# Performance work log

Hardware: AMD Instinct MI355X
Metric: run time of the kernel (lower is better)

Reference implementation:

```python
import jax, jax.numpy as jnp
import numpy as np

NEG_SLOPE = 0.2


def gat_layer(x, src, dst, W, a_src, a_dst, b, n_nodes):
    # x: [N, F_in]; W: [F_in, H*C]; a_src/a_dst: [H, C]; b: [H*C]
    H, C = a_src.shape
    h = (x @ W).reshape(n_nodes, H, C)                    # [N, H, C]
    al_s = jnp.sum(h * a_src, axis=-1)                    # [N, H]
    al_d = jnp.sum(h * a_dst, axis=-1)                    # [N, H]
    e = jax.nn.leaky_relu(al_s[src] + al_d[dst], NEG_SLOPE)  # [E, H]
    # segment softmax over incoming edges of each dst node
    m = jax.ops.segment_max(e, dst, num_segments=n_nodes)   # [N, H]
    e = jnp.exp(e - m[dst])
    s = jax.ops.segment_sum(e, dst, num_segments=n_nodes)   # [N, H]
    alpha = e / (s[dst] + 1e-16)                             # [E, H]
    msg = h[src] * alpha[:, :, None]                         # [E, H, C]
    out = jax.ops.segment_sum(msg, dst, num_segments=n_nodes)
    return out.reshape(n_nodes, H * C) + b


def setup_inputs() -> dict:
    key = jax.random.key(0)
    ks = jax.random.split(key, 16)
    N, E = 50000, 800000
    F_in, Hd, heads, n_cls = 256, 256, 8, 64
    C = Hd // heads
    x = jax.random.normal(ks[0], (N, F_in), dtype=jnp.float32)
    edge_index = jax.random.randint(ks[1], (2, E), 0, N, dtype=jnp.int64)

    def lin(k, fin, fout):
        return jax.random.normal(k, (fin, fout), dtype=jnp.float32) / np.sqrt(fin).astype(np.float32)

    inp = {"x": x, "edge_index": edge_index}
    # layer 1: 256 -> 8 heads x 32
    inp["W1"] = lin(ks[2], F_in, Hd)
    inp["as1"] = jax.random.normal(ks[3], (heads, C), dtype=jnp.float32) * 0.1
    inp["ad1"] = jax.random.normal(ks[4], (heads, C), dtype=jnp.float32) * 0.1
    inp["b1"] = jnp.zeros((Hd,), dtype=jnp.float32)
    # layer 2: 256 -> 8 heads x 32
    inp["W2"] = lin(ks[5], Hd, Hd)
    inp["as2"] = jax.random.normal(ks[6], (heads, C), dtype=jnp.float32) * 0.1
    inp["ad2"] = jax.random.normal(ks[7], (heads, C), dtype=jnp.float32) * 0.1
    inp["b2"] = jnp.zeros((Hd,), dtype=jnp.float32)
    # layer 3: 256 -> 1 head x 64 (num_classes)
    inp["W3"] = lin(ks[8], Hd, n_cls)
    inp["as3"] = jax.random.normal(ks[9], (1, n_cls), dtype=jnp.float32) * 0.1
    inp["ad3"] = jax.random.normal(ks[10], (1, n_cls), dtype=jnp.float32) * 0.1
    inp["b3"] = jnp.zeros((n_cls,), dtype=jnp.float32)
    return inp


def reference(x, edge_index, W1, as1, ad1, b1, W2, as2, ad2, b2, W3, as3, ad3, b3):
    N = x.shape[0]
    # PyG GATConv default add_self_loops=True
    loop = jnp.arange(N, dtype=edge_index.dtype)
    src = jnp.concatenate([edge_index[0], loop])
    dst = jnp.concatenate([edge_index[1], loop])
    h = gat_layer(x, src, dst, W1, as1, ad1, b1, N)
    h = jax.nn.relu(h)  # dropout is identity at inference
    h = gat_layer(h, src, dst, W2, as2, ad2, b2, N)
    h = jax.nn.relu(h)
    out = gat_layer(h, src, dst, W3, as3, ad3, b3, N)
    return out
```

## Files before the change

### kernel.cpp

```cpp
#include <hip/hip_runtime.h>
#include <math.h>

#define NSLOPE 0.2f

typedef __attribute__((ext_vector_type(8))) short bf16x8;
typedef __attribute__((ext_vector_type(8))) unsigned short ushort8;
typedef __attribute__((ext_vector_type(4))) float f32x4;

static __device__ __forceinline__ float leaky(float e) {
    return e > 0.f ? e : NSLOPE * e;
}

static __device__ __forceinline__ float bfu(unsigned short u) {
    return __uint_as_float(((unsigned)u) << 16);
}

static __device__ __forceinline__ unsigned short f2bf_rne(float f) {
    unsigned b = __float_as_uint(f);
    unsigned r = b + 0x7fffu + ((b >> 16) & 1u);
    return (unsigned short)(r >> 16);
}

static __device__ __forceinline__ void split1(float f, unsigned short& hi,
                                              unsigned short& lo) {
    unsigned b = __float_as_uint(f);
    unsigned hb = b & 0xffff0000u;
    hi = (unsigned short)(hb >> 16);
    lo = (unsigned short)(__float_as_uint(f - __uint_as_float(hb)) >> 16);
}


__global__ void k_count(const int* __restrict__ dst, int* __restrict__ cnt, int E) {
    int i = blockIdx.x * blockDim.x + threadIdx.x;
    if (i < E) atomicAdd(&cnt[dst[i]], 1);
}

__global__ void k_scan_local(const int* __restrict__ cnt, int* __restrict__ ptr,
                             int* __restrict__ bsum, int N) {
    __shared__ int sd[256];
    int t = threadIdx.x;
    int i0 = blockIdx.x * 1024 + t * 4;
    int v0 = (i0 + 0 < N) ? cnt[i0 + 0] : 0;
    int v1 = (i0 + 1 < N) ? cnt[i0 + 1] : 0;
    int v2 = (i0 + 2 < N) ? cnt[i0 + 2] : 0;
    int v3 = (i0 + 3 < N) ? cnt[i0 + 3] : 0;
    int ts = v0 + v1 + v2 + v3;
    sd[t] = ts;
    __syncthreads();
    for (int o = 1; o < 256; o <<= 1) {
        int add = (t >= o) ? sd[t - o] : 0;
        __syncthreads();
        sd[t] += add;
        __syncthreads();
    }
    int run = sd[t] - ts;
    if (i0 + 0 < N) ptr[i0 + 0] = run; run += v0;
    if (i0 + 1 < N) ptr[i0 + 1] = run; run += v1;
    if (i0 + 2 < N) ptr[i0 + 2] = run; run += v2;
    if (i0 + 3 < N) ptr[i0 + 3] = run;
    if (t == 255) bsum[blockIdx.x] = sd[255];
}

__global__ void k_scan_add2(int* __restrict__ ptr, const int* __restrict__ bsum,
                            int N, int Et) {
    __shared__ int base;
    const int chunk = blockIdx.x >> 2;
    if (threadIdx.x == 0) {
        int s = 0;
        for (int b = 0; b < chunk; ++b) s += bsum[b];
        base = s;
    }
    __syncthreads();
    int i = blockIdx.x * 256 + threadIdx.x;
    if (i < N) ptr[i] += base;
    else if (i == N) ptr[N] = Et;
}

__global__ void k_copy(int* __restrict__ d, const int* __restrict__ s, int N) {
    int i = blockIdx.x * blockDim.x + threadIdx.x;
    if (i < N) d[i] = s[i];
}

__global__ void k_fillcsr(const int* __restrict__ ei, int* __restrict__ fptr,
                          int* __restrict__ srcs, int E, int Et) {
    int i = blockIdx.x * blockDim.x + threadIdx.x;
    if (i >= Et) return;
    int s, d;
    if (i < E) { s = ei[i]; d = ei[E + i]; }
    else       { s = d = i - E; }
    int pos = atomicAdd(&fptr[d], 1);
    srcs[pos] = s;
}

__global__ __launch_bounds__(256) void k_prep(
    int* __restrict__ cnt, int N,
    const float* __restrict__ x, unsigned short* __restrict__ xhi,
    unsigned short* __restrict__ xlo, int n8,
    const float* __restrict__ W1, unsigned short* __restrict__ w1h, unsigned short* __restrict__ w1l,
    const float* __restrict__ W2, unsigned short* __restrict__ w2h, unsigned short* __restrict__ w2l,
    const float* __restrict__ W3, unsigned short* __restrict__ w3h, unsigned short* __restrict__ w3l,
    int nset, int nsplit) {
    __shared__ float tile[32][33];
    const int b = blockIdx.x;
    const int tid = threadIdx.x;
    if (b < nset) {
        int i = b * 256 + tid;
        if (i < N) cnt[i] = 1;
    } else if (b < nset + nsplit) {
        int i = (b - nset) * 256 + tid;
        if (i < n8) {
            const float4 v0 = *reinterpret_cast<const float4*>(&x[(size_t)i * 8]);
            const float4 v1 = *reinterpret_cast<const float4*>(&x[(size_t)i * 8 + 4]);
            const float f[8] = {v0.x, v0.y, v0.z, v0.w, v1.x, v1.y, v1.z, v1.w};
            ushort8 h, l;
#pragma unroll
            for (int j = 0; j < 8; ++j) {
                unsigned short hj, lj;
                split1(f[j], hj, lj);
                h[j] = hj; l[j] = lj;
            }
            *reinterpret_cast<ushort8*>(&xhi[(size_t)i * 8]) = h;
            *reinterpret_cast<ushort8*>(&xlo[(size_t)i * 8]) = l;
        }
    } else {
        int tb = b - nset - nsplit;
        const float* B; unsigned short *H, *L;
        int M, bx, by;
        if (tb < 64)       { B = W1; H = w1h; L = w1l; M = 256; bx = (tb & 7) * 32; by = (tb >> 3) * 32; }
        else if (tb < 128) { tb -= 64;  B = W2; H = w2h; L = w2l; M = 256; bx = (tb & 7) * 32; by = (tb >> 3) * 32; }
        else               { tb -= 128; B = W3; H = w3h; L = w3l; M = 64;  bx = (tb & 1) * 32; by = (tb >> 1) * 32; }
        constexpr int K = 256;
        const int tx = tid & 31, ty = tid >> 5;
        for (int r = ty; r < 32; r += 8) tile[r][tx] = B[(size_t)(by + r) * M + bx + tx];
        __syncthreads();
        for (int r = ty; r < 32; r += 8) {
            unsigned short h, l;
            split1(tile[tx][r], h, l);
            H[(size_t)(bx + r) * K + by + tx] = h;
            L[(size_t)(bx + r) * K + by + tx] = l;
        }
    }
}

__global__ __launch_bounds__(256) void k_gemm2(const unsigned short* __restrict__ Ahi,
                                               const unsigned short* __restrict__ Alo,
                                               const unsigned short* __restrict__ Whi,
                                               const unsigned short* __restrict__ Wlo,
                                               const float* __restrict__ asrc,
                                               const float* __restrict__ adst,
                                               unsigned short* __restrict__ hb,
                                               float* __restrict__ als,
                                               float* __restrict__ ald,
                                               int N) {
    constexpr int K = 256;
    constexpr int M = 256;
    __shared__ unsigned short Ah[64][36], Al[64][36];
    __shared__ unsigned short Bh[256][36], Bl[256][36];
    const int tid = threadIdx.x;
    const int lane = tid & 63;
    const int wid = tid >> 6;
    const int row0 = blockIdx.x * 64;

    const int sr = tid >> 2;
    const int sk = (tid & 3) << 3;
    const int ga = row0 + sr;
    const size_t gaK = (size_t)ga * K;

    const int wc0 = wid * 64;
    const int fr = lane & 15;
    const int ko = (lane >> 4) * 8;

    f32x4 acc[4][4];
#pragma unroll
    for (int i = 0; i < 4; ++i)
#pragma unroll
        for (int j = 0; j < 4; ++j) acc[i][j] = (f32x4){0.f, 0.f, 0.f, 0.f};

    for (int k0 = 0; k0 < K; k0 += 32) {
        ushort8 ah = {0,0,0,0,0,0,0,0}, al = {0,0,0,0,0,0,0,0};
        if (ga < N) {
            ah = *reinterpret_cast<const ushort8*>(&Ahi[gaK + k0 + sk]);
            al = *reinterpret_cast<const ushort8*>(&Alo[gaK + k0 + sk]);
        }
        *reinterpret_cast<ushort8*>(&Ah[sr][sk]) = ah;
        *reinterpret_cast<ushort8*>(&Al[sr][sk]) = al;
#pragma unroll
        for (int p = 0; p < 4; ++p) {
            const int m = sr + 64 * p;
            const size_t gm = (size_t)m * K + k0 + sk;
            *reinterpret_cast<ushort8*>(&Bh[m][sk]) =
                *reinterpret_cast<const ushort8*>(&Whi[gm]);
            *reinterpret_cast<ushort8*>(&Bl[m][sk]) =
                *reinterpret_cast<const ushort8*>(&Wlo[gm]);
        }
        __syncthreads();

        bf16x8 ahi[4], alo4[4];
#pragma unroll
        for (int i = 0; i < 4; ++i) {
            ahi[i]  = *reinterpret_cast<const bf16x8*>(&Ah[i * 16 + fr][ko]);
            alo4[i] = *reinterpret_cast<const bf16x8*>(&Al[i * 16 + fr][ko]);
        }
#pragma unroll
        for (int j = 0; j < 4; ++j) {
            const bf16x8 bh = *reinterpret_cast<const bf16x8*>(&Bh[wc0 + j * 16 + fr][ko]);
            const bf16x8 bl = *reinterpret_cast<const bf16x8*>(&Bl[wc0 + j * 16 + fr][ko]);
#pragma unroll
            for (int i = 0; i < 4; ++i) {
                acc[i][j] = __builtin_amdgcn_mfma_f32_16x16x32_bf16(ahi[i], bh, acc[i][j], 0, 0, 0);
                acc[i][j] = __builtin_amdgcn_mfma_f32_16x16x32_bf16(ahi[i], bl, acc[i][j], 0, 0, 0);
                acc[i][j] = __builtin_amdgcn_mfma_f32_16x16x32_bf16(alo4[i], bh, acc[i][j], 0, 0, 0);
            }
        }
        __syncthreads();
    }

    const int orow = (lane >> 4) * 4;
    const int ocol = lane & 15;

#pragma unroll
    for (int i = 0; i < 4; ++i) {
#pragma unroll
        for (int r = 0; r < 4; ++r) {
            const int row = row0 + i * 16 + orow + r;
            if (row < N) {
#pragma unroll
                for (int j = 0; j < 4; ++j) {
                    const int col = wc0 + j * 16 + ocol;
                    hb[(size_t)row * M + col] = f2bf_rne(acc[i][j][r]);
                }
            }
        }
    }

    const float as0 = asrc[wc0 + ocol],      as1 = asrc[wc0 + 16 + ocol];
    const float as2 = asrc[wc0 + 32 + ocol], as3 = asrc[wc0 + 48 + ocol];
    const float ad0 = adst[wc0 + ocol],      ad1 = adst[wc0 + 16 + ocol];
    const float ad2 = adst[wc0 + 32 + ocol], ad3 = adst[wc0 + 48 + ocol];
    const int headA = wc0 >> 5, headB = headA + 1;

#pragma unroll
    for (int i = 0; i < 4; ++i) {
#pragma unroll
        for (int r = 0; r < 4; ++r) {
            float psA = acc[i][0][r] * as0 + acc[i][1][r] * as1;
            float pdA = acc[i][0][r] * ad0 + acc[i][1][r] * ad1;
            float psB = acc[i][2][r] * as2 + acc[i][3][r] * as3;
            float pdB = acc[i][2][r] * ad2 + acc[i][3][r] * ad3;
#pragma unroll
            for (int o = 1; o < 16; o <<= 1) {
                psA += __shfl_xor(psA, o);
                pdA += __shfl_xor(pdA, o);
                psB += __shfl_xor(psB, o);
                pdB += __shfl_xor(pdB, o);
            }
            const int row = row0 + i * 16 + orow + r;
            if (ocol == 0 && row < N) {
                als[(size_t)row * 8 + headA] = psA;
                ald[(size_t)row * 8 + headA] = pdA;
                als[(size_t)row * 8 + headB] = psB;
                ald[(size_t)row * 8 + headB] = pdB;
            }
        }
    }
}


template <int HN, int CN>
__global__ __launch_bounds__(256) void k_gemm_s(const unsigned short* __restrict__ Ahi,
                                                const unsigned short* __restrict__ Alo,
                                                const unsigned short* __restrict__ Whi,
                                                const unsigned short* __restrict__ Wlo,
                                                const float* __restrict__ asrc,
                                                const float* __restrict__ adst,
                                                unsigned short* __restrict__ hb,
                                                float* __restrict__ als,
                                                float* __restrict__ ald,
                                                int N) {
    constexpr int K = 256;
    constexpr int M = HN * CN;
    __shared__ unsigned short Ah[64][40], Al[64][40], Bh[64][40], Bl[64][40];
    const int tid = threadIdx.x;
    const int lane = tid & 63;
    const int wid = tid >> 6;
    const int row0 = blockIdx.x * 64;
    const int col0 = blockIdx.y * 64;

    const int sr = tid >> 2;
    const int sk = (tid & 3) << 3;
    const int ga = row0 + sr;
    const size_t gaK = (size_t)ga * K;
    const size_t gcK = (size_t)(col0 + sr) * K;

    const int wr = (wid >> 1) * 32;
    const int wc = (wid & 1) * 32;
    const int fr = lane & 15;
    const int ko = (lane >> 4) * 8;

    f32x4 acc[2][2];
#pragma unroll
    for (int i = 0; i < 2; ++i)
#pragma unroll
        for (int j = 0; j < 2; ++j) acc[i][j] = (f32x4){0.f, 0.f, 0.f, 0.f};

    for (int k0 = 0; k0 < K; k0 += 32) {
        ushort8 ah = {0,0,0,0,0,0,0,0}, al = {0,0,0,0,0,0,0,0};
        if (ga < N) {
            ah = *reinterpret_cast<const ushort8*>(&Ahi[gaK + k0 + sk]);
            al = *reinterpret_cast<const ushort8*>(&Alo[gaK + k0 + sk]);
        }
        const ushort8 bh = *reinterpret_cast<const ushort8*>(&Whi[gcK + k0 + sk]);
        const ushort8 bl = *reinterpret_cast<const ushort8*>(&Wlo[gcK + k0 + sk]);
        *reinterpret_cast<ushort8*>(&Ah[sr][sk]) = ah;
        *reinterpret_cast<ushort8*>(&Al[sr][sk]) = al;
        *reinterpret_cast<ushort8*>(&Bh[sr][sk]) = bh;
        *reinterpret_cast<ushort8*>(&Bl[sr][sk]) = bl;
        __syncthreads();

        bf16x8 ahi[2], alo[2], bhi[2], blo[2];
#pragma unroll
        for (int i = 0; i < 2; ++i) {
            ahi[i] = *reinterpret_cast<const bf16x8*>(&Ah[wr + i * 16 + fr][ko]);
            alo[i] = *reinterpret_cast<const bf16x8*>(&Al[wr + i * 16 + fr][ko]);
        }
#pragma unroll
        for (int j = 0; j < 2; ++j) {
            bhi[j] = *reinterpret_cast<const bf16x8*>(&Bh[wc + j * 16 + fr][ko]);
            blo[j] = *reinterpret_cast<const bf16x8*>(&Bl[wc + j * 16 + fr][ko]);
        }
#pragma unroll
        for (int i = 0; i < 2; ++i)
#pragma unroll
            for (int j = 0; j < 2; ++j) {
                acc[i][j] = __builtin_amdgcn_mfma_f32_16x16x32_bf16(ahi[i], bhi[j], acc[i][j], 0, 0, 0);
                acc[i][j] = __builtin_amdgcn_mfma_f32_16x16x32_bf16(ahi[i], blo[j], acc[i][j], 0, 0, 0);
                acc[i][j] = __builtin_amdgcn_mfma_f32_16x16x32_bf16(alo[i], bhi[j], acc[i][j], 0, 0, 0);
            }
        __syncthreads();
    }

    const int orow = (lane >> 4) * 4;
    const int ocol = lane & 15;

#pragma unroll
    for (int i = 0; i < 2; ++i) {
#pragma unroll
        for (int r = 0; r < 4; ++r) {
            const int row = row0 + wr + i * 16 + orow + r;
            if (row < N) {
#pragma unroll
                for (int j = 0; j < 2; ++j) {
                    const int col = col0 + wc + j * 16 + ocol;
                    hb[(size_t)row * M + col] = f2bf_rne(acc[i][j][r]);
                }
            }
        }
    }

    const int c0 = col0 + wc;
    const float as0 = asrc[c0 + ocol],      as1 = asrc[c0 + 16 + ocol];
    const float ad0 = adst[c0 + ocol],      ad1 = adst[c0 + 16 + ocol];

    {
        __shared__ float part[2][64][2];
#pragma unroll
        for (int i = 0; i < 2; ++i) {
#pragma unroll
            for (int r = 0; r < 4; ++r) {
                float ps = acc[i][0][r] * as0 + acc[i][1][r] * as1;
                float pd = acc[i][0][r] * ad0 + acc[i][1][r] * ad1;
#pragma unroll
                for (int o = 1; o < 16; o <<= 1) {
                    ps += __shfl_xor(ps, o);
                    pd += __shfl_xor(pd, o);
                }
                if (ocol == 0) {
                    const int lr = wr + i * 16 + orow + r;
                    part[wc >> 5][lr][0] = ps;
                    part[wc >> 5][lr][1] = pd;
                }
            }
        }
        __syncthreads();
        if (tid < 64) {
            const int row = row0 + tid;
            if (row < N) {
                als[row] = part[0][tid][0] + part[1][tid][0];
                ald[row] = part[0][tid][1] + part[1][tid][1];
            }
        }
    }
}

template <int HN, int CN, int VEC, int P, bool OSPLIT>
__global__ __launch_bounds__(256) void k_agg6(const unsigned short* __restrict__ hb,
                                              const float* __restrict__ als,
                                              const float* __restrict__ ald,
                                              const int* __restrict__ ptr,
                                              const int* __restrict__ srcs,
                                              const float* __restrict__ bias,
                                              unsigned short* __restrict__ ohi,
                                              unsigned short* __restrict__ olo,
                                              float* __restrict__ out,
                                              int N, int relu) {
    constexpr int HC = HN * CN;
    constexpr int SUBS = 64 / HN;
    constexpr int GB = (SUBS < 16) ? SUBS : 16;
    const int l = threadIdx.x & 63;
    const int n = blockIdx.x * 4 + (threadIdx.x >> 6);
    if (n >= N) return;
    const int beg = ptr[n], end = ptr[n + 1];
    const int hd_e = l % HN;
    const int sub = l / HN;
    const float aldv = ald[(unsigned)n * HN + hd_e];

    float p[P];
    int   sr[P];
    float ssum = 0.f;
#pragma unroll
    for (int b = 0; b < P; ++b) {
        const int j = beg + b * SUBS + sub;
        float pv = 0.f; int s = 0;
        if (j < end) {
            s = srcs[j];
            pv = __expf(leaky(als[(unsigned)s * HN + hd_e] + aldv));
        }
        sr[b] = s; p[b] = pv; ssum += pv;
    }
    for (int j = beg + P * SUBS + sub; j < end; j += SUBS) {
        ssum += __expf(leaky(als[(unsigned)srcs[j] * HN + hd_e] + aldv));
    }
#pragma unroll
    for (int o = HN; o < 64; o <<= 1) ssum += __shfl_xor(ssum, o);
    const float inv = 1.f / (ssum + 1e-16f);

    const int ch = l * VEC;
    const int hl = ch / CN;
    float acc[VEC];
#pragma unroll
    for (int v = 0; v < VEC; ++v) acc[v] = 0.f;

#pragma unroll
    for (int b = 0; b < P; ++b) {
        const int j0 = beg + b * SUBS;
        if (j0 >= end) break;
        const float am = p[b] * inv;
#pragma unroll
        for (int cb = 0; cb < SUBS / GB; ++cb) {
            if (j0 + cb * GB >= end) break;
            float av[GB];
            if constexpr (VEC == 4) {
                ushort4 hv[GB];
#pragma unroll
                for (int c = 0; c < GB; ++c) {
                    const int ce = cb * GB + c;
                    const int s = __shfl(sr[b], ce * HN);
                    av[c] = __shfl(am, ce * HN + hl);
                    hv[c] = *reinterpret_cast<const ushort4*>(&hb[(unsigned)s * HC + ch]);
                }
#pragma unroll
                for (int c = 0; c < GB; ++c) {
                    acc[0] += av[c] * bfu(hv[c].x);
                    acc[1] += av[c] * bfu(hv[c].y);
                    acc[2] += av[c] * bfu(hv[c].z);
                    acc[3] += av[c] * bfu(hv[c].w);
                }
            } else {
                unsigned short hv[GB];
#pragma unroll
                for (int c = 0; c < GB; ++c) {
                    const int ce = cb * GB + c;
                    const int s = __shfl(sr[b], ce * HN);
                    av[c] = __shfl(am, ce * HN + hl);
                    hv[c] = hb[(unsigned)s * HC + ch];
                }
#pragma unroll
                for (int c = 0; c < GB; ++c) acc[0] += av[c] * bfu(hv[c]);
            }
        }
    }
    for (int j0 = beg + P * SUBS; j0 < end; j0 += SUBS) {
        const int j = j0 + sub;
        int sm = 0; float am = 0.f;
        if (j < end) {
            sm = srcs[j];
            am = __expf(leaky(als[(unsigned)sm * HN + hd_e] + aldv)) * inv;
        }
#pragma unroll
        for (int cb = 0; cb < SUBS / GB; ++cb) {
            if (j0 + cb * GB >= end) break;
            float av[GB];
            if constexpr (VEC == 4) {
                ushort4 hv[GB];
#pragma unroll
                for (int c = 0; c < GB; ++c) {
                    const int ce = cb * GB + c;
                    const int s = __shfl(sm, ce * HN);
                    av[c] = __shfl(am, ce * HN + hl);
                    hv[c] = *reinterpret_cast<const ushort4*>(&hb[(unsigned)s * HC + ch]);
                }
#pragma unroll
                for (int c = 0; c < GB; ++c) {
                    acc[0] += av[c] * bfu(hv[c].x);
                    acc[1] += av[c] * bfu(hv[c].y);
                    acc[2] += av[c] * bfu(hv[c].z);
                    acc[3] += av[c] * bfu(hv[c].w);
                }
            } else {
                unsigned short hv[GB];
#pragma unroll
                for (int c = 0; c < GB; ++c) {
                    const int ce = cb * GB + c;
                    const int s = __shfl(sm, ce * HN);
                    av[c] = __shfl(am, ce * HN + hl);
                    hv[c] = hb[(unsigned)s * HC + ch];
                }
#pragma unroll
                for (int c = 0; c < GB; ++c) acc[0] += av[c] * bfu(hv[c]);
            }
        }
    }

#pragma unroll
    for (int v = 0; v < VEC; ++v) {
        float o = acc[v] + bias[ch + v];
        if (relu) o = fmaxf(o, 0.f);
        acc[v] = o;
    }
    if constexpr (OSPLIT) {
        ushort4 ho, lo4;
        unsigned short h0, l0;
        split1(acc[0], h0, l0); ho.x = h0; lo4.x = l0;
        split1(acc[1], h0, l0); ho.y = h0; lo4.y = l0;
        split1(acc[2], h0, l0); ho.z = h0; lo4.z = l0;
        split1(acc[3], h0, l0); ho.w = h0; lo4.w = l0;
        *reinterpret_cast<ushort4*>(&ohi[(unsigned)n * HC + ch]) = ho;
        *reinterpret_cast<ushort4*>(&olo[(unsigned)n * HC + ch]) = lo4;
    } else if constexpr (VEC == 4) {
        float4 vout;
        vout.x = acc[0]; vout.y = acc[1]; vout.z = acc[2]; vout.w = acc[3];
        *reinterpret_cast<float4*>(&out[(unsigned)n * HC + ch]) = vout;
    } else {
        out[(unsigned)n * HC + ch] = acc[0];
    }
}

template <int P>
__global__ __launch_bounds__(256) void k_agg7(const unsigned short* __restrict__ hb,
                                              const float* __restrict__ als,
                                              const float* __restrict__ ald,
                                              const int* __restrict__ ptr,
                                              const int* __restrict__ srcs,
                                              const float* __restrict__ bias,
                                              float* __restrict__ out,
                                              int N) {
    constexpr int HC = 64;
    const int l = threadIdx.x & 63;
    const int n = blockIdx.x * 4 + (threadIdx.x >> 6);
    if (n >= N) return;
    const int beg = ptr[n], end = ptr[n + 1];
    const float aldv = ald[n];

    float p[P];
    int   sr[P];
    float ssum = 0.f;
#pragma unroll
    for (int b = 0; b < P; ++b) {
        const int j = beg + b * 64 + l;
        float pv = 0.f; int s = 0;
        if (j < end) { s = srcs[j]; pv = __expf(leaky(als[s] + aldv)); }
        sr[b] = s; p[b] = pv; ssum += pv;
    }
    for (int j = beg + P * 64 + l; j < end; j += 64)
        ssum += __expf(leaky(als[srcs[j]] + aldv));
#pragma unroll
    for (int o = 1; o < 64; o <<= 1) ssum += __shfl_xor(ssum, o);
    const float inv = 1.f / (ssum + 1e-16f);

    const int grp = l >> 4;
    const int lch = (l & 15) * 4;
    float acc[4] = {0.f, 0.f, 0.f, 0.f};

#pragma unroll
    for (int b = 0; b < P; ++b) {
        const int j0 = beg + b * 64;
        if (j0 >= end) break;
        const float am = p[b] * inv;
        const int ned = min(64, end - j0);
        const int nblk = (ned + 15) >> 4;
        for (int cb = 0; cb < nblk; ++cb) {
            const int e0 = cb * 16 + grp;
            const float a0 = __shfl(am, e0),       a1 = __shfl(am, e0 + 4);
            const float a2 = __shfl(am, e0 + 8),   a3 = __shfl(am, e0 + 12);
            const int   s0 = __shfl(sr[b], e0),      s1 = __shfl(sr[b], e0 + 4);
            const int   s2 = __shfl(sr[b], e0 + 8),  s3 = __shfl(sr[b], e0 + 12);
            const ushort4 h0 = *reinterpret_cast<const ushort4*>(&hb[(unsigned)s0 * HC + lch]);
            const ushort4 h1 = *reinterpret_cast<const ushort4*>(&hb[(unsigned)s1 * HC + lch]);
            const ushort4 h2 = *reinterpret_cast<const ushort4*>(&hb[(unsigned)s2 * HC + lch]);
            const ushort4 h3 = *reinterpret_cast<const ushort4*>(&hb[(unsigned)s3 * HC + lch]);
            acc[0] += a0 * bfu(h0.x) + a1 * bfu(h1.x) + a2 * bfu(h2.x) + a3 * bfu(h3.x);
            acc[1] += a0 * bfu(h0.y) + a1 * bfu(h1.y) + a2 * bfu(h2.y) + a3 * bfu(h3.y);
            acc[2] += a0 * bfu(h0.z) + a1 * bfu(h1.z) + a2 * bfu(h2.z) + a3 * bfu(h3.z);
            acc[3] += a0 * bfu(h0.w) + a1 * bfu(h1.w) + a2 * bfu(h2.w) + a3 * bfu(h3.w);
        }
    }
    for (int j0 = beg + P * 64; j0 < end; j0 += 64) {
        const int j = j0 + l;
        int sm = 0; float am = 0.f;
        if (j < end) { sm = srcs[j]; am = __expf(leaky(als[sm] + aldv)) * inv; }
        const int ned = min(64, end - j0);
        const int nblk = (ned + 15) >> 4;
        for (int cb = 0; cb < nblk; ++cb) {
            const int e0 = cb * 16 + grp;
            const float a0 = __shfl(am, e0),       a1 = __shfl(am, e0 + 4);
            const float a2 = __shfl(am, e0 + 8),   a3 = __shfl(am, e0 + 12);
            const int   s0 = __shfl(sm, e0),       s1 = __shfl(sm, e0 + 4);
            const int   s2 = __shfl(sm, e0 + 8),   s3 = __shfl(sm, e0 + 12);
            const ushort4 h0 = *reinterpret_cast<const ushort4*>(&hb[(unsigned)s0 * HC + lch]);
            const ushort4 h1 = *reinterpret_cast<const ushort4*>(&hb[(unsigned)s1 * HC + lch]);
            const ushort4 h2 = *reinterpret_cast<const ushort4*>(&hb[(unsigned)s2 * HC + lch]);
            const ushort4 h3 = *reinterpret_cast<const ushort4*>(&hb[(unsigned)s3 * HC + lch]);
            acc[0] += a0 * bfu(h0.x) + a1 * bfu(h1.x) + a2 * bfu(h2.x) + a3 * bfu(h3.x);
            acc[1] += a0 * bfu(h0.y) + a1 * bfu(h1.y) + a2 * bfu(h2.y) + a3 * bfu(h3.y);
            acc[2] += a0 * bfu(h0.z) + a1 * bfu(h1.z) + a2 * bfu(h2.z) + a3 * bfu(h3.z);
            acc[3] += a0 * bfu(h0.w) + a1 * bfu(h1.w) + a2 * bfu(h2.w) + a3 * bfu(h3.w);
        }
    }

#pragma unroll
    for (int o = 16; o < 64; o <<= 1) {
#pragma unroll
        for (int v = 0; v < 4; ++v) acc[v] += __shfl_xor(acc[v], o);
    }

    if (l < 16) {
        float4 vout;
        vout.x = acc[0] + bias[lch + 0];
        vout.y = acc[1] + bias[lch + 1];
        vout.z = acc[2] + bias[lch + 2];
        vout.w = acc[3] + bias[lch + 3];
        *reinterpret_cast<float4*>(&out[(size_t)n * HC + lch]) = vout;
    }
}


extern "C" void kernel_launch(void* const* d_in, const int* in_sizes, int n_in,
                              void* d_out, int out_size, void* d_ws, size_t ws_size,
                              hipStream_t stream) {
    const float* x   = (const float*)d_in[0];
    const int*   ei  = (const int*)d_in[1];
    const float* W1  = (const float*)d_in[2];
    const float* as1 = (const float*)d_in[3];
    const float* ad1 = (const float*)d_in[4];
    const float* b1  = (const float*)d_in[5];
    const float* W2  = (const float*)d_in[6];
    const float* as2 = (const float*)d_in[7];
    const float* ad2 = (const float*)d_in[8];
    const float* b2  = (const float*)d_in[9];
    const float* W3  = (const float*)d_in[10];
    const float* as3 = (const float*)d_in[11];
    const float* ad3 = (const float*)d_in[12];
    const float* b3  = (const float*)d_in[13];

    const int F  = 256;
    const int N  = in_sizes[0] / F;
    const int E  = in_sizes[1] / 2;
    const int Et = E + N;

    char* w = (char*)d_ws;
    auto alloc = [&](size_t bytes) {
        char* p = w;
        w += (bytes + 255) & ~(size_t)255;
        return p;
    };
    unsigned short* S0hi = (unsigned short*)alloc((size_t)N * F * 2);
    unsigned short* S0lo = (unsigned short*)alloc((size_t)N * F * 2);
    unsigned short* S1hi = (unsigned short*)alloc((size_t)N * F * 2);
    unsigned short* S1lo = (unsigned short*)alloc((size_t)N * F * 2);
    unsigned short* hB   = (unsigned short*)alloc((size_t)N * F * 2);
    unsigned short* Wt1hi = (unsigned short*)alloc((size_t)256 * 256 * 2);
    unsigned short* Wt1lo = (unsigned short*)alloc((size_t)256 * 256 * 2);
    unsigned short* Wt2hi = (unsigned short*)alloc((size_t)256 * 256 * 2);
    unsigned short* Wt2lo = (unsigned short*)alloc((size_t)256 * 256 * 2);
    unsigned short* Wt3hi = (unsigned short*)alloc((size_t)64 * 256 * 2);
    unsigned short* Wt3lo = (unsigned short*)alloc((size_t)64 * 256 * 2);
    float* als  = (float*)alloc((size_t)N * 8 * 4);
    float* ald  = (float*)alloc((size_t)N * 8 * 4);
    int*   cnt  = (int*)alloc((size_t)N * 4);
    int*   ptr  = (int*)alloc((size_t)(N + 1) * 4);
    int*   fptr = (int*)alloc((size_t)(N + 1) * 4);
    int*   srcs = (int*)alloc((size_t)Et * 4);
    int*   bsum = (int*)alloc(4096);

    const int n8 = N * F / 8;
    const int nset = (N + 255) / 256;
    const int nsplit = (n8 + 255) / 256;
    const int nprep = nset + nsplit + 64 + 64 + 16;

    hipLaunchKernelGGL(k_prep, dim3(nprep), dim3(256), 0, stream,
                       cnt, N, x, S0hi, S0lo, n8,
                       W1, Wt1hi, Wt1lo, W2, Wt2hi, Wt2lo, W3, Wt3hi, Wt3lo,
                       nset, nsplit);

    const int nb = (N + 1023) / 1024;
    hipLaunchKernelGGL(k_count,     dim3((E + 255) / 256),  dim3(256), 0, stream, ei + E, cnt, E);
    hipLaunchKernelGGL(k_scan_local,dim3(nb),               dim3(256), 0, stream, cnt, ptr, bsum, N);
    hipLaunchKernelGGL(k_scan_add2, dim3((N + 256) / 256),  dim3(256), 0, stream, ptr, bsum, N, Et);
    hipLaunchKernelGGL(k_copy,      dim3((N + 255) / 256),  dim3(256), 0, stream, fptr, ptr, N);
    hipLaunchKernelGGL(k_fillcsr,   dim3((Et + 255) / 256), dim3(256), 0, stream, ei, fptr, srcs, E, Et);

    const dim3 gN4((N + 3) / 4);
    const int gx = (N + 63) / 64;

    hipLaunchKernelGGL(k_gemm2, dim3(gx), dim3(256), 0, stream,
                       S0hi, S0lo, Wt1hi, Wt1lo, as1, ad1, hB, als, ald, N);
    hipLaunchKernelGGL((k_agg6<8, 32, 4, 8, true>), gN4, dim3(256), 0, stream,
                       hB, als, ald, ptr, srcs, b1, S1hi, S1lo, nullptr, N, 1);
    hipLaunchKernelGGL(k_gemm2, dim3(gx), dim3(256), 0, stream,
                       S1hi, S1lo, Wt2hi, Wt2lo, as2, ad2, hB, als, ald, N);
    hipLaunchKernelGGL((k_agg6<8, 32, 4, 8, true>), gN4, dim3(256), 0, stream,
                       hB, als, ald, ptr, srcs, b2, S0hi, S0lo, nullptr, N, 1);
    hipLaunchKernelGGL((k_gemm_s<1, 64>), dim3(gx, 1), dim3(256), 0, stream,
                       S0hi, S0lo, Wt3hi, Wt3lo, as3, ad3, hB, als, ald, N);
    hipLaunchKernelGGL((k_agg7<2>), gN4, dim3(256), 0, stream,
                       hB, als, ald, ptr, srcs, b3, (float*)d_out, N);
}
```

Measured before the change: 381.1 us.

## Use 16-byte gathers with half-wave edge split in GAT aggregation; fuse ptr copy

The 8-head aggregation kernel now has each lane load 8 bf16 channels (16 bytes) per source row instead of 4. The wave is split into two 32-lane halves that each process alternate edges, and a cross-half shuffle reduces the partial sums before write-out. This aims to halve the number of gather instructions and raise bytes per load on the irregular neighbor gathers, at the cost of an extra shuffle reduction and idle upper lanes during the store. Separately, the fptr copy is folded into the scan-add kernel, which removes one launch.

```diff
diff --git a/kernel.cpp b/kernel.cpp
--- a/kernel.cpp
+++ b/kernel.cpp
@@ -61,8 +61,8 @@
     if (t == 255) bsum[blockIdx.x] = sd[255];
 }
 
-__global__ void k_scan_add2(int* __restrict__ ptr, const int* __restrict__ bsum,
-                            int N, int Et) {
+__global__ void k_scan_add2(int* __restrict__ ptr, int* __restrict__ fptr,
+                            const int* __restrict__ bsum, int N, int Et) {
     __shared__ int base;
     const int chunk = blockIdx.x >> 2;
     if (threadIdx.x == 0) {
@@ -72,13 +72,13 @@
     }
     __syncthreads();
     int i = blockIdx.x * 256 + threadIdx.x;
-    if (i < N) ptr[i] += base;
-    else if (i == N) ptr[N] = Et;
-}
-
-__global__ void k_copy(int* __restrict__ d, const int* __restrict__ s, int N) {
-    int i = blockIdx.x * blockDim.x + threadIdx.x;
-    if (i < N) d[i] = s[i];
+    if (i < N) {
+        int v = ptr[i] + base;
+        ptr[i] = v;
+        fptr[i] = v;
+    } else if (i == N) {
+        ptr[N] = Et;
+    }
 }
 
 __global__ void k_fillcsr(const int* __restrict__ ei, int* __restrict__ fptr,
@@ -392,8 +392,8 @@
     }
 }
 
-template <int HN, int CN, int VEC, int P, bool OSPLIT>
-__global__ __launch_bounds__(256) void k_agg6(const unsigned short* __restrict__ hb,
+template <int P, bool OSPLIT>
+__global__ __launch_bounds__(256) void k_agg8(const unsigned short* __restrict__ hb,
                                               const float* __restrict__ als,
                                               const float* __restrict__ ald,
                                               const int* __restrict__ ptr,
@@ -403,145 +403,108 @@
                                               unsigned short* __restrict__ olo,
                                               float* __restrict__ out,
                                               int N, int relu) {
-    constexpr int HC = HN * CN;
-    constexpr int SUBS = 64 / HN;
-    constexpr int GB = (SUBS < 16) ? SUBS : 16;
+    constexpr int HC = 256;
     const int l = threadIdx.x & 63;
     const int n = blockIdx.x * 4 + (threadIdx.x >> 6);
     if (n >= N) return;
     const int beg = ptr[n], end = ptr[n + 1];
-    const int hd_e = l % HN;
-    const int sub = l / HN;
-    const float aldv = ald[(unsigned)n * HN + hd_e];
+    const int hd_e = l & 7;
+    const int sub = l >> 3;
+    const float aldv = ald[(unsigned)n * 8 + hd_e];
 
     float p[P];
     int   sr[P];
     float ssum = 0.f;
 #pragma unroll
     for (int b = 0; b < P; ++b) {
-        const int j = beg + b * SUBS + sub;
+        const int j = beg + b * 8 + sub;
         float pv = 0.f; int s = 0;
         if (j < end) {
             s = srcs[j];
-            pv = __expf(leaky(als[(unsigned)s * HN + hd_e] + aldv));
+            pv = __expf(leaky(als[(unsigned)s * 8 + hd_e] + aldv));
         }
         sr[b] = s; p[b] = pv; ssum += pv;
     }
-    for (int j = beg + P * SUBS + sub; j < end; j += SUBS) {
-        ssum += __expf(leaky(als[(unsigned)srcs[j] * HN + hd_e] + aldv));
-    }
-#pragma unroll
-    for (int o = HN; o < 64; o <<= 1) ssum += __shfl_xor(ssum, o);
+    for (int j = beg + P * 8 + sub; j < end; j += 8) {
+        ssum += __expf(leaky(als[(unsigned)srcs[j] * 8 + hd_e] + aldv));
+    }
+#pragma unroll
+    for (int o = 8; o < 64; o <<= 1) ssum += __shfl_xor(ssum, o);
     const float inv = 1.f / (ssum + 1e-16f);
 
-    const int ch = l * VEC;
-    const int hl = ch / CN;
-    float acc[VEC];
-#pragma unroll
-    for (int v = 0; v < VEC; ++v) acc[v] = 0.f;
+    const int grp = l >> 5;
+    const int lch = (l & 31) * 8;
+    const int hl = (l & 31) >> 2;
+    float acc[8];
+#pragma unroll
+    for (int v = 0; v < 8; ++v) acc[v] = 0.f;
 
 #pragma unroll
     for (int b = 0; b < P; ++b) {
-        const int j0 = beg + b * SUBS;
+        const int j0 = beg + b * 8;
         if (j0 >= end) break;
         const float am = p[b] * inv;
-#pragma unroll
-        for (int cb = 0; cb < SUBS / GB; ++cb) {
-            if (j0 + cb * GB >= end) break;
-            float av[GB];
-            if constexpr (VEC == 4) {
-                ushort4 hv[GB];
-#pragma unroll
-                for (int c = 0; c < GB; ++c) {
-                    const int ce = cb * GB + c;
-                    const int s = __shfl(sr[b], ce * HN);
-                    av[c] = __shfl(am, ce * HN + hl);
-                    hv[c] = *reinterpret_cast<const ushort4*>(&hb[(unsigned)s * HC + ch]);
-                }
-#pragma unroll
-                for (int c = 0; c < GB; ++c) {
-                    acc[0] += av[c] * bfu(hv[c].x);
-                    acc[1] += av[c] * bfu(hv[c].y);
-                    acc[2] += av[c] * bfu(hv[c].z);
-                    acc[3] += av[c] * bfu(hv[c].w);
-                }
-            } else {
-                unsigned short hv[GB];
-#pragma unroll
-                for (int c = 0; c < GB; ++c) {
-                    const int ce = cb * GB + c;
-                    const int s = __shfl(sr[b], ce * HN);
-                    av[c] = __shfl(am, ce * HN + hl);
-                    hv[c] = hb[(unsigned)s * HC + ch];
-                }
-#pragma unroll
-                for (int c = 0; c < GB; ++c) acc[0] += av[c] * bfu(hv[c]);
-            }
-        }
-    }
-    for (int j0 = beg + P * SUBS; j0 < end; j0 += SUBS) {
+        float a[4]; int s[4]; ushort8 hv[4];
+#pragma unroll
+        for (int k = 0; k < 4; ++k) {
+            const int ce = 2 * k + grp;
+            a[k] = __shfl(am, ce * 8 + hl);
+            s[k] = __shfl(sr[b], ce * 8);
+            hv[k] = *reinterpret_cast<const ushort8*>(&hb[(unsigned)s[k] * HC + lch]);
+        }
+#pragma unroll
+        for (int k = 0; k < 4; ++k)
+#pragma unroll
+            for (int v = 0; v < 8; ++v) acc[v] += a[k] * bfu(hv[k][v]);
+    }
+    for (int j0 = beg + P * 8; j0 < end; j0 += 8) {
         const int j = j0 + sub;
         int sm = 0; float am = 0.f;
         if (j < end) {
             sm = srcs[j];
-            am = __expf(leaky(als[(unsigned)sm * HN + hd_e] + aldv)) * inv;
-        }
-#pragma unroll
-        for (int cb = 0; cb < SUBS / GB; ++cb) {
-            if (j0 + cb * GB >= end) break;
-            float av[GB];
-            if constexpr (VEC == 4) {
-                ushort4 hv[GB];
-#pragma unroll
-                for (int c = 0; c < GB; ++c) {
-                    const int ce = cb * GB + c;
-                    const int s = __shfl(sm, ce * HN);
-                    av[c] = __shfl(am, ce * HN + hl);
-                    hv[c] = *reinterpret_cast<const ushort4*>(&hb[(unsigned)s * HC + ch]);
-                }
-#pragma unroll
-                for (int c = 0; c < GB; ++c) {
-                    acc[0] += av[c] * bfu(hv[c].x);
-                    acc[1] += av[c] * bfu(hv[c].y);
-                    acc[2] += av[c] * bfu(hv[c].z);
-                    acc[3] += av[c] * bfu(hv[c].w);
-                }
-            } else {
-                unsigned short hv[GB];
-#pragma unroll
-                for (int c = 0; c < GB; ++c) {
-                    const int ce = cb * GB + c;
-                    const int s = __shfl(sm, ce * HN);
-                    av[c] = __shfl(am, ce * HN + hl);
-                    hv[c] = hb[(unsigned)s * HC + ch];
-                }
-#pragma unroll
-                for (int c = 0; c < GB; ++c) acc[0] += av[c] * bfu(hv[c]);
-            }
-        }
-    }
-
-#pragma unroll
-    for (int v = 0; v < VEC; ++v) {
-        float o = acc[v] + bias[ch + v];
-        if (relu) o = fmaxf(o, 0.f);
-        acc[v] = o;
-    }
-    if constexpr (OSPLIT) {
-        ushort4 ho, lo4;
-        unsigned short h0, l0;
-        split1(acc[0], h0, l0); ho.x = h0; lo4.x = l0;
-        split1(acc[1], h0, l0); ho.y = h0; lo4.y = l0;
-        split1(acc[2], h0, l0); ho.z = h0; lo4.z = l0;
-        split1(acc[3], h0, l0); ho.w = h0; lo4.w = l0;
-        *reinterpret_cast<ushort4*>(&ohi[(unsigned)n * HC + ch]) = ho;
-        *reinterpret_cast<ushort4*>(&olo[(unsigned)n * HC + ch]) = lo4;
-    } else if constexpr (VEC == 4) {
-        float4 vout;
-        vout.x = acc[0]; vout.y = acc[1]; vout.z = acc[2]; vout.w = acc[3];
-        *reinterpret_cast<float4*>(&out[(unsigned)n * HC + ch]) = vout;
-    } else {
-        out[(unsigned)n * HC + ch] = acc[0];
+            am = __expf(leaky(als[(unsigned)sm * 8 + hd_e] + aldv)) * inv;
+        }
+        float a[4]; int s[4]; ushort8 hv[4];
+#pragma unroll
+        for (int k = 0; k < 4; ++k) {
+            const int ce = 2 * k + grp;
+            a[k] = __shfl(am, ce * 8 + hl);
+            s[k] = __shfl(sm, ce * 8);
+            hv[k] = *reinterpret_cast<const ushort8*>(&hb[(unsigned)s[k] * HC + lch]);
+        }
+#pragma unroll
+        for (int k = 0; k < 4; ++k)
+#pragma unroll
+            for (int v = 0; v < 8; ++v) acc[v] += a[k] * bfu(hv[k][v]);
+    }
+
+#pragma unroll
+    for (int v = 0; v < 8; ++v) acc[v] += __shfl_xor(acc[v], 32);
+
+    if (l < 32) {
+#pragma unroll
+        for (int v = 0; v < 8; ++v) {
+            float o = acc[v] + bias[lch + v];
+            if (relu) o = fmaxf(o, 0.f);
+            acc[v] = o;
+        }
+        if constexpr (OSPLIT) {
+            ushort8 ho, lo8;
+#pragma unroll
+            for (int v = 0; v < 8; ++v) {
+                unsigned short h0, l0;
+                split1(acc[v], h0, l0);
+                ho[v] = h0; lo8[v] = l0;
+            }
+            *reinterpret_cast<ushort8*>(&ohi[(unsigned)n * HC + lch]) = ho;
+            *reinterpret_cast<ushort8*>(&olo[(unsigned)n * HC + lch]) = lo8;
+        } else {
+            float4 v0, v1;
+            v0.x = acc[0]; v0.y = acc[1]; v0.z = acc[2]; v0.w = acc[3];
+            v1.x = acc[4]; v1.y = acc[5]; v1.z = acc[6]; v1.w = acc[7];
+            *reinterpret_cast<float4*>(&out[(unsigned)n * HC + lch]) = v0;
+            *reinterpret_cast<float4*>(&out[(unsigned)n * HC + lch + 4]) = v1;
+        }
     }
 }
 
@@ -705,8 +668,7 @@
     const int nb = (N + 1023) / 1024;
     hipLaunchKernelGGL(k_count,     dim3((E + 255) / 256),  dim3(256), 0, stream, ei + E, cnt, E);
     hipLaunchKernelGGL(k_scan_local,dim3(nb),               dim3(256), 0, stream, cnt, ptr, bsum, N);
-    hipLaunchKernelGGL(k_scan_add2, dim3((N + 256) / 256),  dim3(256), 0, stream, ptr, bsum, N, Et);
-    hipLaunchKernelGGL(k_copy,      dim3((N + 255) / 256),  dim3(256), 0, stream, fptr, ptr, N);
+    hipLaunchKernelGGL(k_scan_add2, dim3((N + 256) / 256),  dim3(256), 0, stream, ptr, fptr, bsum, N, Et);
     hipLaunchKernelGGL(k_fillcsr,   dim3((Et + 255) / 256), dim3(256), 0, stream, ei, fptr, srcs, E, Et);
 
     const dim3 gN4((N + 3) / 4);
@@ -714,11 +676,11 @@
 
     hipLaunchKernelGGL(k_gemm2, dim3(gx), dim3(256), 0, stream,
                        S0hi, S0lo, Wt1hi, Wt1lo, as1, ad1, hB, als, ald, N);
-    hipLaunchKernelGGL((k_agg6<8, 32, 4, 8, true>), gN4, dim3(256), 0, stream,
+    hipLaunchKernelGGL((k_agg8<8, true>), gN4, dim3(256), 0, stream,
                        hB, als, ald, ptr, srcs, b1, S1hi, S1lo, nullptr, N, 1);
     hipLaunchKernelGGL(k_gemm2, dim3(gx), dim3(256), 0, stream,
                        S1hi, S1lo, Wt2hi, Wt2lo, as2, ad2, hB, als, ald, N);
-    hipLaunchKernelGGL((k_agg6<8, 32, 4, 8, true>), gN4, dim3(256), 0, stream,
+    hipLaunchKernelGGL((k_agg8<8, true>), gN4, dim3(256), 0, stream,
                        hB, als, ald, ptr, srcs, b2, S0hi, S0lo, nullptr, N, 1);
     hipLaunchKernelGGL((k_gemm_s<1, 64>), dim3(gx, 1), dim3(256), 0, stream,
                        S0hi, S0lo, Wt3hi, Wt3lo, as3, ad3, hB, als, ald, N);
```

Result: slower. 392.2 us (+2.9%).
